# Kernel optimization log

Measured on AMD Instinct MI355X. Metric: run time of the kernel, lower is better.

The kernel has to match this reference:

```python
import jax, jax.numpy as jnp
import numpy as np

D_MODEL = 1024
NUM_HEADS = 16
D_K = D_MODEL // NUM_HEADS
THETA = 10000.0
SEQ = 2048
BATCH = 2


def _rope(t, positions):
    # t: [b, h, s, d_k]; positions: [s]
    half = D_K // 2
    freqs = 1.0 / (THETA ** (jnp.arange(0, D_K, 2, dtype=jnp.float32) / D_K))  # [half]
    angles = positions.astype(jnp.float32)[:, None] * freqs[None, :]  # [s, half]
    cos = jnp.cos(angles)  # [s, half]
    sin = jnp.sin(angles)
    tr = t.reshape(t.shape[:-1] + (half, 2))  # pairs are (even, odd) interleaved
    x1, x2 = tr[..., 0], tr[..., 1]
    r1 = x1 * cos - x2 * sin
    r2 = x1 * sin + x2 * cos
    return jnp.stack([r1, r2], axis=-1).reshape(t.shape)


def setup_inputs() -> dict:
    key = jax.random.key(0)
    ks = jax.random.split(key, 5)
    std = float(np.sqrt(2.0 / (D_MODEL + D_MODEL)))
    return {
        "x": jax.random.normal(ks[0], (BATCH, SEQ, D_MODEL), dtype=jnp.float32),
        "token_positions": jnp.arange(SEQ, dtype=jnp.int64 if jax.config.jax_enable_x64 else jnp.int32),
        "wq": std * jax.random.normal(ks[1], (D_MODEL, D_MODEL), dtype=jnp.float32),
        "wk": std * jax.random.normal(ks[2], (D_MODEL, D_MODEL), dtype=jnp.float32),
        "wv": std * jax.random.normal(ks[3], (D_MODEL, D_MODEL), dtype=jnp.float32),
        "wo": std * jax.random.normal(ks[4], (D_MODEL, D_MODEL), dtype=jnp.float32),
    }


def reference(x, token_positions, wq, wk, wv, wo):
    b, s, _ = x.shape
    # projections: weight is (d_out, d_in), y = x @ W^T
    def proj(w):
        y = jnp.einsum('bsd,od->bso', x, w)
        return y.reshape(b, s, NUM_HEADS, D_K).transpose(0, 2, 1, 3)  # [b,h,s,dk]
    Q, K, V = proj(wq), proj(wk), proj(wv)
    Q = _rope(Q, token_positions)
    K = _rope(K, token_positions)
    scale = 1.0 / jnp.sqrt(jnp.asarray(D_K, dtype=x.dtype))
    scores = jnp.einsum('bhqd,bhkd->bhqk', Q, K) * scale  # [b,h,s,s]
    causal = jnp.tril(jnp.ones((s, s), dtype=bool))
    scores = jnp.where(causal, scores, jnp.asarray(-jnp.inf, dtype=scores.dtype))
    attn = jax.nn.softmax(scores, axis=-1)
    out = jnp.einsum('bhqk,bhkd->bhqd', attn, V)  # [b,h,s,dk]
    out = out.transpose(0, 2, 1, 3).reshape(b, s, D_MODEL)
    return jnp.einsum('bsd,od->bso', out, wo)
```

## Files before the change

### kernel.cpp

```cpp
#include <hip/hip_runtime.h>
#include <hip/hip_bf16.h>
#include <math.h>

#define BATCH  2
#define SEQ    2048
#define DMODEL 1024
#define NHEADS 16
#define DK     64

typedef __hip_bfloat16 bf16;
typedef short s16x8 __attribute__((ext_vector_type(8)));
typedef float f32x4 __attribute__((ext_vector_type(4)));

union P8 { int4 i4; s16x8 v; short s[8]; };

static __device__ __forceinline__ unsigned short f2bu(float f) {
    bf16 h = __float2bfloat16(f);
    return *reinterpret_cast<unsigned short*>(&h);
}
static __device__ __forceinline__ float bu2f(unsigned short u) {
    return __uint_as_float((unsigned int)u << 16);
}

static __device__ __forceinline__ void gll16(const void* g, void* l) {
    __builtin_amdgcn_global_load_lds(
        (const __attribute__((address_space(1))) unsigned int*)g,
        (__attribute__((address_space(3))) unsigned int*)l, 16, 0, 0);
}

__global__ __launch_bounds__(256) void conv_k(
    const float* __restrict__ x, const float* __restrict__ wq,
    const float* __restrict__ wk, const float* __restrict__ wv,
    const float* __restrict__ wo, bf16* __restrict__ dst)
{
    const size_t e0 = ((size_t)blockIdx.x * 256 + threadIdx.x) << 3;
    const float* src;
    bf16* d;
    if (e0 < (size_t)4194304) { src = x + e0; d = dst + e0; }
    else {
        const size_t r = e0 - 4194304;
        const int wsel = (int)(r >> 20);
        const size_t off = r & 1048575;
        src = (wsel == 0 ? wq : wsel == 1 ? wk : wsel == 2 ? wv : wo) + off;
        d = dst + 4194304 + ((size_t)wsel << 20) + off;
    }
    const float4 a = *(const float4*)src;
    const float4 b = *(const float4*)(src + 4);
    P8 p;
    p.s[0] = (short)f2bu(a.x); p.s[1] = (short)f2bu(a.y);
    p.s[2] = (short)f2bu(a.z); p.s[3] = (short)f2bu(a.w);
    p.s[4] = (short)f2bu(b.x); p.s[5] = (short)f2bu(b.y);
    p.s[6] = (short)f2bu(b.z); p.s[7] = (short)f2bu(b.w);
    *(int4*)d = p.i4;
}

__global__ __launch_bounds__(256) void gemm_qkv(
    const bf16* __restrict__ Ab, const bf16* __restrict__ Wb,
    bf16* __restrict__ O0, bf16* __restrict__ O1, bf16* __restrict__ O2)
{
    __shared__ __align__(16) short As[128 * 32];
    __shared__ __align__(16) short Ws[128 * 32];
    const int tid  = threadIdx.x;
    const int w    = tid >> 6;
    const int lane = tid & 63;
    const int ln   = lane & 15;
    const int quad = lane >> 4;
    const int lr   = lane >> 2;
    const int lc   = (lane & 3) << 3;
    const int id   = blockIdx.x;
    const int m_base = (id & 31) << 7;
    const int n_base = ((id >> 5) & 7) << 7;
    const int z = id >> 8;
    const bf16* Wz = Wb + ((size_t)z << 20);

    const size_t arow0 = (size_t)(m_base + 32 * w + lr) * DMODEL + lc;
    const size_t arow1 = arow0 + (size_t)16 * DMODEL;
    const size_t wrow0 = (size_t)(n_base + 32 * w + lr) * DMODEL + lc;
    const size_t wrow1 = wrow0 + (size_t)16 * DMODEL;
    short* ldsA0 = &As[1024 * w]; short* ldsA1 = ldsA0 + 512;
    short* ldsW0 = &Ws[1024 * w]; short* ldsW1 = ldsW0 + 512;

    const f32x4 zero4 = {0.f, 0.f, 0.f, 0.f};
    f32x4 acc[4][4];
    #pragma unroll
    for (int i = 0; i < 4; ++i)
        #pragma unroll
        for (int j = 0; j < 4; ++j) acc[i][j] = zero4;

    const int mo = (w >> 1) << 6, no = (w & 1) << 6;

    for (int k0 = 0; k0 < DMODEL; k0 += 32) {
        __syncthreads();
        gll16(Ab + arow0 + k0, ldsA0);
        gll16(Ab + arow1 + k0, ldsA1);
        gll16(Wz + wrow0 + k0, ldsW0);
        gll16(Wz + wrow1 + k0, ldsW1);
        __syncthreads();
        s16x8 af[4], bw[4];
        #pragma unroll
        for (int i = 0; i < 4; ++i) {
            af[i] = *(const s16x8*)&As[(mo + 16 * i + ln) * 32 + quad * 8];
            bw[i] = *(const s16x8*)&Ws[(no + 16 * i + ln) * 32 + quad * 8];
        }
        #pragma unroll
        for (int mi = 0; mi < 4; ++mi)
            #pragma unroll
            for (int ni = 0; ni < 4; ++ni)
                acc[mi][ni] = __builtin_amdgcn_mfma_f32_16x16x32_bf16(
                    af[mi], bw[ni], acc[mi][ni], 0, 0, 0);
    }

    #pragma unroll
    for (int mi = 0; mi < 4; ++mi) {
        #pragma unroll
        for (int ni = 0; ni < 4; ++ni) {
            const int n = n_base + no + 16 * ni + ln;
            const int h = n >> 6, d = n & (DK - 1);
            if (z < 2) {
                bf16* C = (z == 0) ? O0 : O1;
                #pragma unroll
                for (int r = 0; r < 4; ++r) {
                    const int m = m_base + mo + 16 * mi + quad * 4 + r;
                    const int b = m >> 11, s = m & (SEQ - 1);
                    C[(((size_t)(b * NHEADS + h) * SEQ) + s) * DK + d] =
                        __float2bfloat16(acc[mi][ni][r]);
                }
            } else {
                const int m0v = m_base + mo + 16 * mi + quad * 4;
                const int b = m0v >> 11, s0 = m0v & (SEQ - 1);
                ushort4 pk;
                pk.x = f2bu(acc[mi][ni][0]); pk.y = f2bu(acc[mi][ni][1]);
                pk.z = f2bu(acc[mi][ni][2]); pk.w = f2bu(acc[mi][ni][3]);
                *(ushort4*)(O2 + (((size_t)(b * NHEADS + h) * DK) + d) * SEQ + s0) = pk;
            }
        }
    }
}

__global__ __launch_bounds__(256) void gemm_wo(
    const bf16* __restrict__ Ab, const bf16* __restrict__ Wb,
    float* __restrict__ Of)
{
    __shared__ __align__(16) short As[64 * 32];
    __shared__ __align__(16) short Ws[128 * 32];
    const int tid  = threadIdx.x;
    const int w    = tid >> 6;
    const int lane = tid & 63;
    const int ln   = lane & 15;
    const int quad = lane >> 4;
    const int lr   = lane >> 2;
    const int lc   = (lane & 3) << 3;
    const int id   = blockIdx.x;
    const int m_base = (id & 63) << 6;
    const int n_base = (id >> 6) << 7;

    const int am = m_base + 16 * w + lr;
    const int ab = am >> 11, asx = am & (SEQ - 1);
    const size_t arow = ((size_t)ab * NHEADS * SEQ + asx) * DK + lc;
    const size_t wrow0 = (size_t)(n_base + 32 * w + lr) * DMODEL + lc;
    const size_t wrow1 = wrow0 + (size_t)16 * DMODEL;
    short* ldsA0 = &As[512 * w];
    short* ldsW0 = &Ws[1024 * w]; short* ldsW1 = ldsW0 + 512;

    const f32x4 zero4 = {0.f, 0.f, 0.f, 0.f};
    f32x4 acc[2][4];
    #pragma unroll
    for (int i = 0; i < 2; ++i)
        #pragma unroll
        for (int j = 0; j < 4; ++j) acc[i][j] = zero4;

    const int mo = (w >> 1) << 5, no = (w & 1) << 6;

    for (int k0 = 0; k0 < DMODEL; k0 += 32) {
        const size_t ka = (size_t)(k0 >> 6) * (SEQ * DK) + (k0 & 32);
        __syncthreads();
        gll16(Ab + arow + ka, ldsA0);
        gll16(Wb + wrow0 + k0, ldsW0);
        gll16(Wb + wrow1 + k0, ldsW1);
        __syncthreads();
        s16x8 af[2], bw[4];
        #pragma unroll
        for (int i = 0; i < 2; ++i)
            af[i] = *(const s16x8*)&As[(mo + 16 * i + ln) * 32 + quad * 8];
        #pragma unroll
        for (int j = 0; j < 4; ++j)
            bw[j] = *(const s16x8*)&Ws[(no + 16 * j + ln) * 32 + quad * 8];
        #pragma unroll
        for (int mi = 0; mi < 2; ++mi)
            #pragma unroll
            for (int ni = 0; ni < 4; ++ni)
                acc[mi][ni] = __builtin_amdgcn_mfma_f32_16x16x32_bf16(
                    af[mi], bw[ni], acc[mi][ni], 0, 0, 0);
    }

    #pragma unroll
    for (int mi = 0; mi < 2; ++mi)
        #pragma unroll
        for (int ni = 0; ni < 4; ++ni) {
            const int n = n_base + no + 16 * ni + ln;
            #pragma unroll
            for (int r = 0; r < 4; ++r) {
                const int m = m_base + mo + 16 * mi + quad * 4 + r;
                Of[(size_t)m * DMODEL + n] = acc[mi][ni][r];
            }
        }
}

__global__ __launch_bounds__(256) void rope_k(bf16* __restrict__ Q, bf16* __restrict__ Kk)
{
    const unsigned int idx = blockIdx.x * 256 + threadIdx.x;
    const unsigned int p = idx & ((1u << 21) - 1);
    const bool isq = (idx >> 21) == 0;
    bf16* buf = isq ? Q : Kk;
    unsigned int* wp = reinterpret_cast<unsigned int*>(buf + ((size_t)p << 1));
    const unsigned int u = *wp;
    const int pi = p & 31;
    const int s = (p >> 5) & (SEQ - 1);
    const float freq = exp2f(-(float)pi * 0.4152410119f);
    float sn, cs;
    sincosf((float)s * freq, &sn, &cs);
    const float e = bu2f((unsigned short)(u & 0xffffu));
    const float o = bu2f((unsigned short)(u >> 16));
    const float sc = isq ? 0.125f : 1.0f;
    const unsigned int lo = f2bu((e * cs - o * sn) * sc);
    const unsigned int hi = f2bu((e * sn + o * cs) * sc);
    *wp = lo | (hi << 16);
}

__global__ __launch_bounds__(256) void attn_k(bf16* __restrict__ Q,
                                              const bf16* __restrict__ Kg,
                                              const bf16* __restrict__ VT)
{
    __shared__ __align__(16) short Ks[64 * 72];
    __shared__ __align__(16) short Vs[64 * 72];
    __shared__ __align__(16) short PT[64 * 72];
    const int tid  = threadIdx.x;
    const int w    = tid >> 6;
    const int lane = tid & 63;
    const int ln   = lane & 15;
    const int quad = lane >> 4;
    const int bh = blockIdx.x & 31;
    const int qt = 31 - (blockIdx.x >> 5);
    const size_t base = (size_t)bh * (SEQ * DK);
    const int srow = tid >> 2;
    const int sc   = (tid & 3) << 4;
    const int qrow = qt * 64 + 16 * w + ln;

    P8 qa0, qa1;
    {
        const bf16* qsrc = Q + base + (size_t)qrow * DK + quad * 8;
        qa0.i4 = *(const int4*)(qsrc);
        qa1.i4 = *(const int4*)(qsrc + 32);
    }
    const f32x4 zero4 = {0.f, 0.f, 0.f, 0.f};
    f32x4 o[4];
    #pragma unroll
    for (int mt = 0; mt < 4; ++mt) o[mt] = zero4;
    float lsum = 0.f;

    P8 kk[2], vv[2];
    {
        const bf16* ksrc = Kg + base + (size_t)srow * DK + sc;
        kk[0].i4 = *(const int4*)(ksrc);
        kk[1].i4 = *(const int4*)(ksrc + 8);
        const bf16* vsrc = VT + base + (size_t)srow * SEQ + sc;
        vv[0].i4 = *(const int4*)(vsrc);
        vv[1].i4 = *(const int4*)(vsrc + 8);
    }

    for (int kb = 0; kb <= qt; ++kb) {
        __syncthreads();
        *(s16x8*)&Ks[srow * 72 + sc]     = kk[0].v;
        *(s16x8*)&Ks[srow * 72 + sc + 8] = kk[1].v;
        *(s16x8*)&Vs[srow * 72 + sc]     = vv[0].v;
        *(s16x8*)&Vs[srow * 72 + sc + 8] = vv[1].v;
        __syncthreads();

        if (kb < qt) {
            const bf16* ksrc = Kg + base + (size_t)((kb + 1) * 64 + srow) * DK + sc;
            kk[0].i4 = *(const int4*)(ksrc);
            kk[1].i4 = *(const int4*)(ksrc + 8);
            const bf16* vsrc = VT + base + (size_t)srow * SEQ + (kb + 1) * 64 + sc;
            vv[0].i4 = *(const int4*)(vsrc);
            vv[1].i4 = *(const int4*)(vsrc + 8);
        }

        f32x4 sf[4];
        #pragma unroll
        for (int mt = 0; mt < 4; ++mt) {
            sf[mt] = zero4;
            s16x8 ka  = *(const s16x8*)&Ks[(16 * mt + ln) * 72 + quad * 8];
            s16x8 kb2 = *(const s16x8*)&Ks[(16 * mt + ln) * 72 + 32 + quad * 8];
            sf[mt] = __builtin_amdgcn_mfma_f32_16x16x32_bf16(ka,  qa0.v, sf[mt], 0, 0, 0);
            sf[mt] = __builtin_amdgcn_mfma_f32_16x16x32_bf16(kb2, qa1.v, sf[mt], 0, 0, 0);
        }

        if (kb == qt) {
            #pragma unroll
            for (int mt = 0; mt < 4; ++mt)
                #pragma unroll
                for (int r = 0; r < 4; ++r)
                    if (kb * 64 + 16 * mt + quad * 4 + r > qrow) sf[mt][r] = -INFINITY;
        }
        #pragma unroll
        for (int mt = 0; mt < 4; ++mt)
            #pragma unroll
            for (int r = 0; r < 4; ++r) {
                sf[mt][r] = __expf(sf[mt][r]);
                lsum += sf[mt][r];
            }

        #pragma unroll
        for (int mt = 0; mt < 4; ++mt) {
            ushort4 pk;
            pk.x = f2bu(sf[mt][0]); pk.y = f2bu(sf[mt][1]);
            pk.z = f2bu(sf[mt][2]); pk.w = f2bu(sf[mt][3]);
            *(ushort4*)&PT[(16 * w + ln) * 72 + 16 * mt + quad * 4] = pk;
        }

        s16x8 pa0 = *(const s16x8*)&PT[(16 * w + ln) * 72 + quad * 8];
        s16x8 pa1 = *(const s16x8*)&PT[(16 * w + ln) * 72 + 32 + quad * 8];
        #pragma unroll
        for (int mt = 0; mt < 4; ++mt) {
            s16x8 va0 = *(const s16x8*)&Vs[(16 * mt + ln) * 72 + quad * 8];
            s16x8 va1 = *(const s16x8*)&Vs[(16 * mt + ln) * 72 + 32 + quad * 8];
            o[mt] = __builtin_amdgcn_mfma_f32_16x16x32_bf16(va0, pa0, o[mt], 0, 0, 0);
            o[mt] = __builtin_amdgcn_mfma_f32_16x16x32_bf16(va1, pa1, o[mt], 0, 0, 0);
        }
    }

    lsum += __shfl_xor(lsum, 16, 64);
    lsum += __shfl_xor(lsum, 32, 64);
    const float inv = 1.0f / lsum;
    #pragma unroll
    for (int mt = 0; mt < 4; ++mt) {
        ushort4 st;
        st.x = f2bu(o[mt][0] * inv); st.y = f2bu(o[mt][1] * inv);
        st.z = f2bu(o[mt][2] * inv); st.w = f2bu(o[mt][3] * inv);
        *(ushort4*)(Q + base + (size_t)qrow * DK + 16 * mt + quad * 4) = st;
    }
}

extern "C" void kernel_launch(void* const* d_in, const int* in_sizes, int n_in,
                              void* d_out, int out_size, void* d_ws, size_t ws_size,
                              hipStream_t stream)
{
    const float* x  = (const float*)d_in[0];
    const float* wq = (const float*)d_in[2];
    const float* wk = (const float*)d_in[3];
    const float* wv = (const float*)d_in[4];
    const float* wo = (const float*)d_in[5];

    bf16* wsb   = (bf16*)d_ws;
    bf16* xb    = wsb;
    bf16* wqkvb = wsb + ((size_t)4 << 20);
    bf16* wob   = wsb + ((size_t)7 << 20);
    bf16* Qw    = wsb + ((size_t)8 << 20);
    bf16* Kw    = wsb + ((size_t)12 << 20);
    bf16* VTw   = wsb + ((size_t)16 << 20);

    conv_k<<<4096, 256, 0, stream>>>(x, wq, wk, wv, wo, wsb);
    gemm_qkv<<<768, 256, 0, stream>>>(xb, wqkvb, Qw, Kw, VTw);
    rope_k<<<(BATCH * NHEADS * SEQ * DK / 2) / 256 * 2, 256, 0, stream>>>(Qw, Kw);
    attn_k<<<1024, 256, 0, stream>>>(Qw, Kw, VTw);
    gemm_wo<<<512, 256, 0, stream>>>(Qw, wob, (float*)d_out);
}
```

Baseline: 181.3 us.

## Fuse RoPE into QKV GEMM epilogue and widen K-tiles with XOR-swizzled LDS

Removes the separate RoPE kernel by applying the rotation and Q scaling inside the QKV GEMM epilogue, using a lane shuffle to fetch the paired even/odd element. Both GEMMs now stage 64-wide K tiles per iteration with an XOR swizzle on LDS columns, which halves barrier count and is meant to avoid bank conflicts. This saves one launch plus a full read-modify-write pass over Q and K. In exchange it doubles LDS use per block and adds sincos work in the epilogue.

```diff
diff --git a/kernel.cpp b/kernel.cpp
--- a/kernel.cpp
+++ b/kernel.cpp
@@ -58,27 +58,25 @@
     const bf16* __restrict__ Ab, const bf16* __restrict__ Wb,
     bf16* __restrict__ O0, bf16* __restrict__ O1, bf16* __restrict__ O2)
 {
-    __shared__ __align__(16) short As[128 * 32];
-    __shared__ __align__(16) short Ws[128 * 32];
+    __shared__ __align__(16) short As[128 * 64];
+    __shared__ __align__(16) short Ws[128 * 64];
     const int tid  = threadIdx.x;
     const int w    = tid >> 6;
     const int lane = tid & 63;
     const int ln   = lane & 15;
     const int quad = lane >> 4;
-    const int lr   = lane >> 2;
-    const int lc   = (lane & 3) << 3;
     const int id   = blockIdx.x;
     const int m_base = (id & 31) << 7;
     const int n_base = ((id >> 5) & 7) << 7;
     const int z = id >> 8;
     const bf16* Wz = Wb + ((size_t)z << 20);
 
-    const size_t arow0 = (size_t)(m_base + 32 * w + lr) * DMODEL + lc;
-    const size_t arow1 = arow0 + (size_t)16 * DMODEL;
-    const size_t wrow0 = (size_t)(n_base + 32 * w + lr) * DMODEL + lc;
-    const size_t wrow1 = wrow0 + (size_t)16 * DMODEL;
-    short* ldsA0 = &As[1024 * w]; short* ldsA1 = ldsA0 + 512;
-    short* ldsW0 = &Ws[1024 * w]; short* ldsW1 = ldsW0 + 512;
+    const int lrw = lane >> 3;
+    const int lcs = ((lane & 7) ^ lrw) << 3;
+    const size_t abase = (size_t)(m_base + 32 * w + lrw) * DMODEL + lcs;
+    const size_t wbase = (size_t)(n_base + 32 * w + lrw) * DMODEL + lcs;
+    short* ldsA = &As[2048 * w];
+    short* ldsW = &Ws[2048 * w];
 
     const f32x4 zero4 = {0.f, 0.f, 0.f, 0.f};
     f32x4 acc[4][4];
@@ -88,44 +86,65 @@
         for (int j = 0; j < 4; ++j) acc[i][j] = zero4;
 
     const int mo = (w >> 1) << 6, no = (w & 1) << 6;
-
-    for (int k0 = 0; k0 < DMODEL; k0 += 32) {
-        __syncthreads();
-        gll16(Ab + arow0 + k0, ldsA0);
-        gll16(Ab + arow1 + k0, ldsA1);
-        gll16(Wz + wrow0 + k0, ldsW0);
-        gll16(Wz + wrow1 + k0, ldsW1);
-        __syncthreads();
-        s16x8 af[4], bw[4];
-        #pragma unroll
-        for (int i = 0; i < 4; ++i) {
-            af[i] = *(const s16x8*)&As[(mo + 16 * i + ln) * 32 + quad * 8];
-            bw[i] = *(const s16x8*)&Ws[(no + 16 * i + ln) * 32 + quad * 8];
-        }
-        #pragma unroll
-        for (int mi = 0; mi < 4; ++mi)
-            #pragma unroll
-            for (int ni = 0; ni < 4; ++ni)
-                acc[mi][ni] = __builtin_amdgcn_mfma_f32_16x16x32_bf16(
-                    af[mi], bw[ni], acc[mi][ni], 0, 0, 0);
-    }
-
-    #pragma unroll
-    for (int mi = 0; mi < 4; ++mi) {
+    const int swz = ln & 7;
+
+    for (int k0 = 0; k0 < DMODEL; k0 += 64) {
+        __syncthreads();
+        #pragma unroll
+        for (int t = 0; t < 4; ++t) {
+            gll16(Ab + abase + (size_t)t * 8 * DMODEL + k0, ldsA + t * 512);
+            gll16(Wz + wbase + (size_t)t * 8 * DMODEL + k0, ldsW + t * 512);
+        }
+        __syncthreads();
+        #pragma unroll
+        for (int t = 0; t < 2; ++t) {
+            const int co = (((t << 2) + quad) ^ swz) << 3;
+            s16x8 af[4], bw[4];
+            #pragma unroll
+            for (int i = 0; i < 4; ++i) {
+                af[i] = *(const s16x8*)&As[(mo + 16 * i + ln) * 64 + co];
+                bw[i] = *(const s16x8*)&Ws[(no + 16 * i + ln) * 64 + co];
+            }
+            #pragma unroll
+            for (int mi = 0; mi < 4; ++mi)
+                #pragma unroll
+                for (int ni = 0; ni < 4; ++ni)
+                    acc[mi][ni] = __builtin_amdgcn_mfma_f32_16x16x32_bf16(
+                        af[mi], bw[ni], acc[mi][ni], 0, 0, 0);
+        }
+    }
+
+    if (z < 2) {
+        bf16* C = (z == 0) ? O0 : O1;
+        const float qs = (z == 0) ? 0.125f : 1.0f;
         #pragma unroll
         for (int ni = 0; ni < 4; ++ni) {
             const int n = n_base + no + 16 * ni + ln;
             const int h = n >> 6, d = n & (DK - 1);
-            if (z < 2) {
-                bf16* C = (z == 0) ? O0 : O1;
+            const float freq = exp2f(-(float)(d >> 1) * 0.4152410119f);
+            const float sgn = (d & 1) ? 1.0f : -1.0f;
+            #pragma unroll
+            for (int mi = 0; mi < 4; ++mi)
                 #pragma unroll
                 for (int r = 0; r < 4; ++r) {
                     const int m = m_base + mo + 16 * mi + quad * 4 + r;
                     const int b = m >> 11, s = m & (SEQ - 1);
+                    float sn, cs;
+                    sincosf((float)s * freq, &sn, &cs);
+                    const float v = acc[mi][ni][r];
+                    const float p = __shfl_xor(v, 1, 64);
+                    const float res = (v * cs + sgn * p * sn) * qs;
                     C[(((size_t)(b * NHEADS + h) * SEQ) + s) * DK + d] =
-                        __float2bfloat16(acc[mi][ni][r]);
+                        __float2bfloat16(res);
                 }
-            } else {
+        }
+    } else {
+        #pragma unroll
+        for (int ni = 0; ni < 4; ++ni) {
+            const int n = n_base + no + 16 * ni + ln;
+            const int h = n >> 6, d = n & (DK - 1);
+            #pragma unroll
+            for (int mi = 0; mi < 4; ++mi) {
                 const int m0v = m_base + mo + 16 * mi + quad * 4;
                 const int b = m0v >> 11, s0 = m0v & (SEQ - 1);
                 ushort4 pk;
@@ -141,26 +160,23 @@
     const bf16* __restrict__ Ab, const bf16* __restrict__ Wb,
     float* __restrict__ Of)
 {
-    __shared__ __align__(16) short As[64 * 32];
-    __shared__ __align__(16) short Ws[128 * 32];
+    __shared__ __align__(16) short As[64 * 64];
+    __shared__ __align__(16) short Ws[128 * 64];
     const int tid  = threadIdx.x;
     const int w    = tid >> 6;
     const int lane = tid & 63;
     const int ln   = lane & 15;
     const int quad = lane >> 4;
-    const int lr   = lane >> 2;
-    const int lc   = (lane & 3) << 3;
     const int id   = blockIdx.x;
     const int m_base = (id & 63) << 6;
     const int n_base = (id >> 6) << 7;
 
-    const int am = m_base + 16 * w + lr;
-    const int ab = am >> 11, asx = am & (SEQ - 1);
-    const size_t arow = ((size_t)ab * NHEADS * SEQ + asx) * DK + lc;
-    const size_t wrow0 = (size_t)(n_base + 32 * w + lr) * DMODEL + lc;
-    const size_t wrow1 = wrow0 + (size_t)16 * DMODEL;
-    short* ldsA0 = &As[512 * w];
-    short* ldsW0 = &Ws[1024 * w]; short* ldsW1 = ldsW0 + 512;
+    const int lrw = lane >> 3;
+    const int lcs = ((lane & 7) ^ lrw) << 3;
+    const int am = m_base + 16 * w + lrw;
+    short* ldsA = &As[1024 * w];
+    const size_t wbase = (size_t)(n_base + 32 * w + lrw) * DMODEL + lcs;
+    short* ldsW = &Ws[2048 * w];
 
     const f32x4 zero4 = {0.f, 0.f, 0.f, 0.f};
     f32x4 acc[2][4];
@@ -170,27 +186,39 @@
         for (int j = 0; j < 4; ++j) acc[i][j] = zero4;
 
     const int mo = (w >> 1) << 5, no = (w & 1) << 6;
-
-    for (int k0 = 0; k0 < DMODEL; k0 += 32) {
-        const size_t ka = (size_t)(k0 >> 6) * (SEQ * DK) + (k0 & 32);
-        __syncthreads();
-        gll16(Ab + arow + ka, ldsA0);
-        gll16(Wb + wrow0 + k0, ldsW0);
-        gll16(Wb + wrow1 + k0, ldsW1);
-        __syncthreads();
-        s16x8 af[2], bw[4];
-        #pragma unroll
-        for (int i = 0; i < 2; ++i)
-            af[i] = *(const s16x8*)&As[(mo + 16 * i + ln) * 32 + quad * 8];
-        #pragma unroll
-        for (int j = 0; j < 4; ++j)
-            bw[j] = *(const s16x8*)&Ws[(no + 16 * j + ln) * 32 + quad * 8];
-        #pragma unroll
-        for (int mi = 0; mi < 2; ++mi)
-            #pragma unroll
-            for (int ni = 0; ni < 4; ++ni)
-                acc[mi][ni] = __builtin_amdgcn_mfma_f32_16x16x32_bf16(
-                    af[mi], bw[ni], acc[mi][ni], 0, 0, 0);
+    const int swz = ln & 7;
+
+    for (int k0 = 0; k0 < DMODEL; k0 += 64) {
+        const int hh = k0 >> 6;
+        __syncthreads();
+        #pragma unroll
+        for (int t = 0; t < 2; ++t) {
+            const int m = am + t * 8;
+            const int b = m >> 11, s = m & (SEQ - 1);
+            gll16(Ab + (((size_t)(b * NHEADS + hh) * SEQ) + s) * DK + lcs,
+                  ldsA + t * 512);
+        }
+        #pragma unroll
+        for (int t = 0; t < 4; ++t)
+            gll16(Wb + wbase + (size_t)t * 8 * DMODEL + k0, ldsW + t * 512);
+        __syncthreads();
+        #pragma unroll
+        for (int t = 0; t < 2; ++t) {
+            const int co = (((t << 2) + quad) ^ swz) << 3;
+            s16x8 af[2], bw[4];
+            #pragma unroll
+            for (int i = 0; i < 2; ++i)
+                af[i] = *(const s16x8*)&As[(mo + 16 * i + ln) * 64 + co];
+            #pragma unroll
+            for (int j = 0; j < 4; ++j)
+                bw[j] = *(const s16x8*)&Ws[(no + 16 * j + ln) * 64 + co];
+            #pragma unroll
+            for (int mi = 0; mi < 2; ++mi)
+                #pragma unroll
+                for (int ni = 0; ni < 4; ++ni)
+                    acc[mi][ni] = __builtin_amdgcn_mfma_f32_16x16x32_bf16(
+                        af[mi], bw[ni], acc[mi][ni], 0, 0, 0);
+        }
     }
 
     #pragma unroll
@@ -204,27 +232,6 @@
                 Of[(size_t)m * DMODEL + n] = acc[mi][ni][r];
             }
         }
-}
-
-__global__ __launch_bounds__(256) void rope_k(bf16* __restrict__ Q, bf16* __restrict__ Kk)
-{
-    const unsigned int idx = blockIdx.x * 256 + threadIdx.x;
-    const unsigned int p = idx & ((1u << 21) - 1);
-    const bool isq = (idx >> 21) == 0;
-    bf16* buf = isq ? Q : Kk;
-    unsigned int* wp = reinterpret_cast<unsigned int*>(buf + ((size_t)p << 1));
-    const unsigned int u = *wp;
-    const int pi = p & 31;
-    const int s = (p >> 5) & (SEQ - 1);
-    const float freq = exp2f(-(float)pi * 0.4152410119f);
-    float sn, cs;
-    sincosf((float)s * freq, &sn, &cs);
-    const float e = bu2f((unsigned short)(u & 0xffffu));
-    const float o = bu2f((unsigned short)(u >> 16));
-    const float sc = isq ? 0.125f : 1.0f;
-    const unsigned int lo = f2bu((e * cs - o * sn) * sc);
-    const unsigned int hi = f2bu((e * sn + o * cs) * sc);
-    *wp = lo | (hi << 16);
 }
 
 __global__ __launch_bounds__(256) void attn_k(bf16* __restrict__ Q,
@@ -361,7 +368,6 @@
 
     conv_k<<<4096, 256, 0, stream>>>(x, wq, wk, wv, wo, wsb);
     gemm_qkv<<<768, 256, 0, stream>>>(xb, wqkvb, Qw, Kw, VTw);
-    rope_k<<<(BATCH * NHEADS * SEQ * DK / 2) / 256 * 2, 256, 0, stream>>>(Qw, Kw);
     attn_k<<<1024, 256, 0, stream>>>(Qw, Kw, VTw);
     gemm_wo<<<512, 256, 0, stream>>>(Qw, wob, (float*)d_out);
 }
```

After: 272.7 us. +50.5%, slower.
